# Kernel optimization log

Hardware: AMD Instinct MI355X
Metric: run time of the kernel (lower is better)

The kernel has to match this reference:

```python
import jax, jax.numpy as jnp
import numpy as np

NUM_CAPSULE = 128   # must equal steps (seq_len) for the reshape in the original code
DIM_CAPSULE = 64
ROUTINGS = 3
EPS = 1e-7          # K.epsilon()


def pos_emb(x):
    """Sinusoidal position embedding added to x over its last two dims [..., S, D].
    Matches the Keras code: evens use sin(pos/10000^(2k/D)), odds use cos with the
    same frequency (odds-1 == 2k), interleaved via stack+reshape."""
    S, D = x.shape[-2], x.shape[-1]
    pos = jnp.arange(S, dtype=x.dtype)[:, None]                      # [S,1]
    inv_freq = 1.0 / jnp.power(10000.0, (2.0 * jnp.arange(D // 2, dtype=x.dtype)) / D)
    ang = pos * inv_freq[None, :]                                    # [S, D/2]
    pe = jnp.stack([jnp.sin(ang), jnp.cos(ang)], axis=-1).reshape(S, D)
    return x + pe


def squash(s):
    ss = jnp.sum(s * s, axis=-1, keepdims=True)
    scale = ss / (1.0 + ss) / jnp.sqrt(ss + EPS)
    return scale * s


def setup_inputs() -> dict:
    key = jax.random.key(0)
    k1, k2 = jax.random.split(key)
    B, steps, in_dim = 32, 128, 256
    u_vecs = jax.random.normal(k1, (B, steps, in_dim), dtype=jnp.float32)
    mask = jnp.ones((B, steps), dtype=jnp.float32)
    # glorot_uniform for capsule kernel (1, in_dim, dim_capsule)
    lim = float(np.sqrt(6.0 / (in_dim + DIM_CAPSULE)))
    W = jax.random.uniform(k2, (1, in_dim, DIM_CAPSULE), jnp.float32, -lim, lim)
    return {"u_vecs": u_vecs, "mask": mask, "W": W}


def reference(u_vecs, mask, W):
    B, steps, in_dim = u_vecs.shape
    N, D = NUM_CAPSULE, DIM_CAPSULE  # N == steps by construction
    # share_weights branch: tile W across steps, permute, add PE, flatten to a conv1d
    # kernel of width 1 -> a plain [in_dim, steps*D] projection matrix.
    tmp = jnp.transpose(jnp.broadcast_to(W, (steps, in_dim, D)), (1, 0, 2))  # [in_dim, steps, D]
    kernel = pos_emb(tmp).reshape(in_dim, steps * D)                          # [in_dim, steps*D]
    u_hat = jnp.einsum('bsi,io->bso', u_vecs, kernel)                         # [B, steps, steps*D]
    u_hat = pos_emb(u_hat)
    u_hat = u_hat.reshape(B, steps, N, D).transpose(0, 2, 1, 3)               # [B, N, In, D]
    b = jnp.zeros((B, N, steps), dtype=u_hat.dtype)                           # routing logits
    m = mask[:, None, :]                                                      # [B, 1, In]
    outputs = None
    for i in range(ROUTINGS):
        # softmax over the num_capsule axis (permute->softmax(-1)->permute in Keras)
        c = jax.nn.softmax(b, axis=1) * m                                     # [B, N, In]
        outputs = squash(jnp.einsum('bni,bnid->bnd', c, u_hat))               # [B, N, D]
        if i < ROUTINGS - 1:
            b = jnp.einsum('bnd,bnid->bni', outputs, u_hat)                   # agreement
    return outputs
```

## Files before the change

### kernel.cpp

```cpp
#include <hip/hip_runtime.h>
#include <math.h>

#define NB 32
#define NS 128
#define NI 256
#define NC 128
#define ND 64

#define L4 9.210340371976184f

__global__ __launch_bounds__(256) void k_prep(const float* __restrict__ u,
                                              const float* __restrict__ W,
                                              float* __restrict__ M,
                                              float* __restrict__ U,
                                              float* __restrict__ PE1) {
    int blk = blockIdx.x;
    int t = threadIdx.x;
    if (blk < 1024) {
        int row = blk * 4 + (t >> 6);
        int d = t & 63;
        const float* ur = u + row * NI;
        float acc = 0.f, rs = 0.f;
#pragma unroll 4
        for (int i = 0; i < NI; ++i) {
            float v = ur[i];
            acc = fmaf(v, W[i * ND + d], acc);
            rs += v;
        }
        M[row * ND + d] = acc;
        if (d == 0) U[row] = rs;
    } else {
        int idx = (blk - 1024) * 256 + t;
        int n = idx >> 6, d = idx & 63;
        float ang = (float)n * __expf(-L4 * (float)(d >> 1) * (1.f / 32.f));
        float sv, cv;
        __sincosf(ang, &sv, &cv);
        PE1[idx] = (d & 1) ? cv : sv;
    }
}

__global__ __launch_bounds__(256, 4) void kR(const float* __restrict__ M,
                                             const float* __restrict__ U,
                                             const float* __restrict__ PE1,
                                             const float* __restrict__ cg,
                                             const float* __restrict__ mask,
                                             float* __restrict__ og,
                                             float* __restrict__ bl,
                                             int first, int last) {
    int bp = blockIdx.x;
    int n  = bp & 127;
    int b0 = (bp >> 7) * 2;
    int t  = threadIdx.x;

    __shared__ float4 redw[2][4][16];
    __shared__ float4 outs4[2][16];
    __shared__ float  tpar[2][2];
    __shared__ float  sc2[2][2];
    __shared__ float  red2[2][NS * 17];

    int dq = t & 15, sq = t >> 4;
    int s0 = sq * 8;

    const float* cr0 = first ? (mask + b0 * NS)
                             : (cg + ((size_t)(b0 * NC + n)) * NS);
    const float* cr1 = first ? (mask + (b0 + 1) * NS)
                             : (cg + ((size_t)((b0 + 1) * NC + n)) * NS);

    float4 c0a = *(const float4*)(cr0 + s0);
    float4 c0b = *(const float4*)(cr0 + s0 + 4);
    float4 c1a = *(const float4*)(cr1 + s0);
    float4 c1b = *(const float4*)(cr1 + s0 + 4);

    int k2 = n * 32 + dq * 2;
    float g0 = __expf(-L4 * (float)k2 * (1.f / 4096.f));
    float g1 = __expf(-L4 * (float)(k2 + 1) * (1.f / 4096.f));
    float sg0 = __sinf(g0), cg0 = __cosf(g0);
    float sg1 = __sinf(g1), cg1 = __cosf(g1);
    float sa = __sinf((float)s0 * g0), ca = __cosf((float)s0 * g0);
    float sb = __sinf((float)s0 * g1), cb = __cosf((float)s0 * g1);

    const float4* M4a = (const float4*)(M + (size_t)(b0 * NS) * ND) + dq;
    const float4* M4b = M4a + NS * 16;
    float4 va[8], vb[8];
    float4 acc0 = make_float4(0.f, 0.f, 0.f, 0.f);
    float4 acc1 = make_float4(0.f, 0.f, 0.f, 0.f);
#pragma unroll
    for (int i = 0; i < 8; ++i) {
        int s = s0 + i;
        float4 m0 = M4a[s * 16];
        float4 m1 = M4b[s * 16];
        float cc0 = (i < 4) ? ((const float*)&c0a)[i & 3] : ((const float*)&c0b)[i & 3];
        float cc1 = (i < 4) ? ((const float*)&c1a)[i & 3] : ((const float*)&c1b)[i & 3];
        float4 u0, u1;
        u0.x = m0.x + sa; u0.y = m0.y + ca; u0.z = m0.z + sb; u0.w = m0.w + cb;
        u1.x = m1.x + sa; u1.y = m1.y + ca; u1.z = m1.z + sb; u1.w = m1.w + cb;
        va[i] = u0; vb[i] = u1;
        acc0.x = fmaf(cc0, u0.x, acc0.x);
        acc0.y = fmaf(cc0, u0.y, acc0.y);
        acc0.z = fmaf(cc0, u0.z, acc0.z);
        acc0.w = fmaf(cc0, u0.w, acc0.w);
        acc1.x = fmaf(cc1, u1.x, acc1.x);
        acc1.y = fmaf(cc1, u1.y, acc1.y);
        acc1.z = fmaf(cc1, u1.z, acc1.z);
        acc1.w = fmaf(cc1, u1.w, acc1.w);
        float nsa = fmaf(sa, cg0, ca * sg0);
        float nca = fmaf(ca, cg0, -sa * sg0);
        sa = nsa; ca = nca;
        float nsb = fmaf(sb, cg1, cb * sg1);
        float ncb = fmaf(cb, cg1, -sb * sg1);
        sb = nsb; cb = ncb;
    }
#pragma unroll
    for (int o = 16; o <= 32; o <<= 1) {
        acc0.x += __shfl_xor(acc0.x, o); acc0.y += __shfl_xor(acc0.y, o);
        acc0.z += __shfl_xor(acc0.z, o); acc0.w += __shfl_xor(acc0.w, o);
        acc1.x += __shfl_xor(acc1.x, o); acc1.y += __shfl_xor(acc1.y, o);
        acc1.z += __shfl_xor(acc1.z, o); acc1.w += __shfl_xor(acc1.w, o);
    }
    if ((t & 48) == 0) {
        int w = t >> 6;
        redw[0][w][dq] = acc0;
        redw[1][w][dq] = acc1;
    }
    {
        int bh = t >> 7, s = t & 127;
        const float* cr = bh ? cr1 : cr0;
        float p = cr[s] * U[(b0 + bh) * NS + s];
#pragma unroll
        for (int o = 32; o > 0; o >>= 1) p += __shfl_xor(p, o);
        if ((t & 63) == 0) tpar[bh][(t >> 6) & 1] = p;
    }
    __syncthreads();

    if (t < 32) {
        int bh = t >> 4, q = t & 15;
        float4 r0 = redw[bh][0][q], r1 = redw[bh][1][q];
        float4 r2 = redw[bh][2][q], r3 = redw[bh][3][q];
        float4 o;
        o.x = r0.x + r1.x + r2.x + r3.x;
        o.y = r0.y + r1.y + r2.y + r3.y;
        o.z = r0.z + r1.z + r2.z + r3.z;
        o.w = r0.w + r1.w + r2.w + r3.w;
        float T2 = tpar[bh][0] + tpar[bh][1];
        float4 p14 = ((const float4*)PE1)[n * 16 + q];
        o.x = fmaf(p14.x, T2, o.x);
        o.y = fmaf(p14.y, T2, o.y);
        o.z = fmaf(p14.z, T2, o.z);
        o.w = fmaf(p14.w, T2, o.w);
        if (first) { o.x *= (1.f / 128.f); o.y *= (1.f / 128.f);
                     o.z *= (1.f / 128.f); o.w *= (1.f / 128.f); }
        outs4[bh][q] = o;
        float ssq = o.x * o.x + o.y * o.y + o.z * o.z + o.w * o.w;
        float ppu = o.x * p14.x + o.y * p14.y + o.z * p14.z + o.w * p14.w;
#pragma unroll
        for (int o2 = 1; o2 <= 8; o2 <<= 1) {
            ssq += __shfl_xor(ssq, o2);
            ppu += __shfl_xor(ppu, o2);
        }
        if (q == 0) {
            sc2[bh][0] = ssq / (1.f + ssq) * rsqrtf(ssq + 1e-7f);
            sc2[bh][1] = ppu;
        }
    }
    __syncthreads();

    if (last) {
        if (t < 32) {
            int bh = t >> 4, q = t & 15;
            float sc = sc2[bh][0];
            float4 o = outs4[bh][q];
            o.x *= sc; o.y *= sc; o.z *= sc; o.w *= sc;
            ((float4*)og)[((b0 + bh) * NC + n) * 16 + q] = o;
        }
        return;
    }

    float4 oa = outs4[0][dq], ob = outs4[1][dq];
#pragma unroll
    for (int i = 0; i < 8; ++i) {
        int s = s0 + i;
        float4 v0 = va[i], v1 = vb[i];
        red2[0][s * 17 + dq] = v0.x * oa.x + v0.y * oa.y + v0.z * oa.z + v0.w * oa.w;
        red2[1][s * 17 + dq] = v1.x * ob.x + v1.y * ob.y + v1.z * ob.z + v1.w * ob.w;
    }
    __syncthreads();
    {
        int bh = t >> 7, s = t & 127;
        const float* r = &red2[bh][s * 17];
        float sum = 0.f;
#pragma unroll
        for (int q = 0; q < 16; ++q) sum += r[q];
        bl[((b0 + bh) * NC + n) * NS + s] =
            sc2[bh][0] * (sum + sc2[bh][1] * U[(b0 + bh) * NS + s]);
    }
}

__global__ __launch_bounds__(256) void kS(const float* __restrict__ bl,
                                          const float* __restrict__ mask,
                                          float* __restrict__ c) {
    int blk = blockIdx.x;
    int b = blk >> 4, s0 = (blk & 15) * 8;
    int t = threadIdx.x;

    __shared__ float tl[NC][9];
    __shared__ float pr[32][9];
    __shared__ float ps[32][9];
    __shared__ float itot[8], msk[8];

    if (t < 8) msk[t] = mask[b * NS + s0 + t];
#pragma unroll
    for (int i = 0; i < 4; ++i) {
        int idx = i * 256 + t;
        int n = idx >> 3, si = idx & 7;
        tl[n][si] = bl[(b * NC + n) * NS + s0 + si];
    }
    __syncthreads();

    int si = t & 7, ch = t >> 3;
    float mx = -1e30f;
#pragma unroll
    for (int j = 0; j < 4; ++j) mx = fmaxf(mx, tl[ch * 4 + j][si]);
    pr[ch][si] = mx;
    __syncthreads();

    mx = pr[0][si];
#pragma unroll
    for (int jc = 1; jc < 32; ++jc) mx = fmaxf(mx, pr[jc][si]);
    float sm = 0.f;
#pragma unroll
    for (int j = 0; j < 4; ++j) {
        float e = __expf(tl[ch * 4 + j][si] - mx);
        tl[ch * 4 + j][si] = e;
        sm += e;
    }
    ps[ch][si] = sm;
    __syncthreads();

    if (t < 8) {
        float tot = 0.f;
#pragma unroll
        for (int jc = 0; jc < 32; ++jc) tot += ps[jc][t];
        itot[t] = msk[t] / tot;
    }
    __syncthreads();

#pragma unroll
    for (int i = 0; i < 4; ++i) {
        int idx = i * 256 + t;
        int n = idx >> 3, sj = idx & 7;
        c[(b * NC + n) * NS + s0 + sj] = tl[n][sj] * itot[sj];
    }
}

extern "C" void kernel_launch(void* const* d_in, const int* in_sizes, int n_in,
                              void* d_out, int out_size, void* d_ws, size_t ws_size,
                              hipStream_t stream) {
    const float* u    = (const float*)d_in[0];
    const float* mask = (const float*)d_in[1];
    const float* W    = (const float*)d_in[2];
    float* out = (float*)d_out;

    float* ws  = (float*)d_ws;
    float* M   = ws;
    float* U   = M + NB * NS * ND;
    float* PE1 = U + NB * NS;
    float* c   = PE1 + NC * ND;
    float* bl  = c + NB * NC * NS;

    k_prep<<<1056, 256, 0, stream>>>(u, W, M, U, PE1);

    kR<<<2048, 256, 0, stream>>>(M, U, PE1, c, mask, out, bl, 1, 0);
    kS<<<512, 256, 0, stream>>>(bl, mask, c);
    kR<<<2048, 256, 0, stream>>>(M, U, PE1, c, mask, out, bl, 0, 0);
    kS<<<512, 256, 0, stream>>>(bl, mask, c);
    kR<<<2048, 256, 0, stream>>>(M, U, PE1, c, mask, out, bl, 0, 1);
}
```

Before: 115.0 us.

## Fuse routing softmax into routing kernel and transpose logits layout

```diff
diff --git a/kernel.cpp b/kernel.cpp
--- a/kernel.cpp
+++ b/kernel.cpp
@@ -42,35 +42,57 @@
 __global__ __launch_bounds__(256, 4) void kR(const float* __restrict__ M,
                                              const float* __restrict__ U,
                                              const float* __restrict__ PE1,
-                                             const float* __restrict__ cg,
                                              const float* __restrict__ mask,
+                                             const float* __restrict__ blr,
+                                             float* __restrict__ blw,
                                              float* __restrict__ og,
-                                             float* __restrict__ bl,
                                              int first, int last) {
     int bp = blockIdx.x;
     int n  = bp & 127;
     int b0 = (bp >> 7) * 2;
     int t  = threadIdx.x;
 
+    __shared__ float  cs[2][NS];
     __shared__ float4 redw[2][4][16];
     __shared__ float4 outs4[2][16];
     __shared__ float  tpar[2][2];
     __shared__ float  sc2[2][2];
     __shared__ float  red2[2][NS * 17];
 
+    {
+        int bh = t >> 7, s = t & 127;
+        int b = b0 + bh;
+        float uu = U[b * NS + s];
+        float cv;
+        if (first) {
+            cv = mask[b * NS + s];
+        } else {
+            const float4* row = (const float4*)(blr + ((size_t)(b * NS + s)) * NC);
+            float mx = -1e30f;
+#pragma unroll 8
+            for (int i = 0; i < 32; ++i) {
+                float4 v = row[i];
+                mx = fmaxf(mx, fmaxf(fmaxf(v.x, v.y), fmaxf(v.z, v.w)));
+            }
+            float den = 0.f;
+#pragma unroll 8
+            for (int i = 0; i < 32; ++i) {
+                float4 v = row[i];
+                den += __expf(v.x - mx) + __expf(v.y - mx) +
+                       __expf(v.z - mx) + __expf(v.w - mx);
+            }
+            float blv = blr[((size_t)(b * NS + s)) * NC + n];
+            cv = __expf(blv - mx) * mask[b * NS + s] / den;
+        }
+        cs[bh][s] = cv;
+        float p = cv * uu;
+#pragma unroll
+        for (int o = 32; o > 0; o >>= 1) p += __shfl_xor(p, o);
+        if ((t & 63) == 0) tpar[bh][(t >> 6) & 1] = p;
+    }
+
     int dq = t & 15, sq = t >> 4;
     int s0 = sq * 8;
-
-    const float* cr0 = first ? (mask + b0 * NS)
-                             : (cg + ((size_t)(b0 * NC + n)) * NS);
-    const float* cr1 = first ? (mask + (b0 + 1) * NS)
-                             : (cg + ((size_t)((b0 + 1) * NC + n)) * NS);
-
-    float4 c0a = *(const float4*)(cr0 + s0);
-    float4 c0b = *(const float4*)(cr0 + s0 + 4);
-    float4 c1a = *(const float4*)(cr1 + s0);
-    float4 c1b = *(const float4*)(cr1 + s0 + 4);
-
     int k2 = n * 32 + dq * 2;
     float g0 = __expf(-L4 * (float)k2 * (1.f / 4096.f));
     float g1 = __expf(-L4 * (float)(k2 + 1) * (1.f / 4096.f));
@@ -78,6 +100,7 @@
     float sg1 = __sinf(g1), cg1 = __cosf(g1);
     float sa = __sinf((float)s0 * g0), ca = __cosf((float)s0 * g0);
     float sb = __sinf((float)s0 * g1), cb = __cosf((float)s0 * g1);
+    __syncthreads();
 
     const float4* M4a = (const float4*)(M + (size_t)(b0 * NS) * ND) + dq;
     const float4* M4b = M4a + NS * 16;
@@ -89,8 +112,7 @@
         int s = s0 + i;
         float4 m0 = M4a[s * 16];
         float4 m1 = M4b[s * 16];
-        float cc0 = (i < 4) ? ((const float*)&c0a)[i & 3] : ((const float*)&c0b)[i & 3];
-        float cc1 = (i < 4) ? ((const float*)&c1a)[i & 3] : ((const float*)&c1b)[i & 3];
+        float cc0 = cs[0][s], cc1 = cs[1][s];
         float4 u0, u1;
         u0.x = m0.x + sa; u0.y = m0.y + ca; u0.z = m0.z + sb; u0.w = m0.w + cb;
         u1.x = m1.x + sa; u1.y = m1.y + ca; u1.z = m1.z + sb; u1.w = m1.w + cb;
@@ -121,14 +143,6 @@
         int w = t >> 6;
         redw[0][w][dq] = acc0;
         redw[1][w][dq] = acc1;
-    }
-    {
-        int bh = t >> 7, s = t & 127;
-        const float* cr = bh ? cr1 : cr0;
-        float p = cr[s] * U[(b0 + bh) * NS + s];
-#pragma unroll
-        for (int o = 32; o > 0; o >>= 1) p += __shfl_xor(p, o);
-        if ((t & 63) == 0) tpar[bh][(t >> 6) & 1] = p;
     }
     __syncthreads();
 
@@ -186,69 +200,13 @@
     __syncthreads();
     {
         int bh = t >> 7, s = t & 127;
+        int b = b0 + bh;
         const float* r = &red2[bh][s * 17];
         float sum = 0.f;
 #pragma unroll
         for (int q = 0; q < 16; ++q) sum += r[q];
-        bl[((b0 + bh) * NC + n) * NS + s] =
-            sc2[bh][0] * (sum + sc2[bh][1] * U[(b0 + bh) * NS + s]);
-    }
-}
-
-__global__ __launch_bounds__(256) void kS(const float* __restrict__ bl,
-                                          const float* __restrict__ mask,
-                                          float* __restrict__ c) {
-    int blk = blockIdx.x;
-    int b = blk >> 4, s0 = (blk & 15) * 8;
-    int t = threadIdx.x;
-
-    __shared__ float tl[NC][9];
-    __shared__ float pr[32][9];
-    __shared__ float ps[32][9];
-    __shared__ float itot[8], msk[8];
-
-    if (t < 8) msk[t] = mask[b * NS + s0 + t];
-#pragma unroll
-    for (int i = 0; i < 4; ++i) {
-        int idx = i * 256 + t;
-        int n = idx >> 3, si = idx & 7;
-        tl[n][si] = bl[(b * NC + n) * NS + s0 + si];
-    }
-    __syncthreads();
-
-    int si = t & 7, ch = t >> 3;
-    float mx = -1e30f;
-#pragma unroll
-    for (int j = 0; j < 4; ++j) mx = fmaxf(mx, tl[ch * 4 + j][si]);
-    pr[ch][si] = mx;
-    __syncthreads();
-
-    mx = pr[0][si];
-#pragma unroll
-    for (int jc = 1; jc < 32; ++jc) mx = fmaxf(mx, pr[jc][si]);
-    float sm = 0.f;
-#pragma unroll
-    for (int j = 0; j < 4; ++j) {
-        float e = __expf(tl[ch * 4 + j][si] - mx);
-        tl[ch * 4 + j][si] = e;
-        sm += e;
-    }
-    ps[ch][si] = sm;
-    __syncthreads();
-
-    if (t < 8) {
-        float tot = 0.f;
-#pragma unroll
-        for (int jc = 0; jc < 32; ++jc) tot += ps[jc][t];
-        itot[t] = msk[t] / tot;
-    }
-    __syncthreads();
-
-#pragma unroll
-    for (int i = 0; i < 4; ++i) {
-        int idx = i * 256 + t;
-        int n = idx >> 3, sj = idx & 7;
-        c[(b * NC + n) * NS + s0 + sj] = tl[n][sj] * itot[sj];
+        blw[((size_t)(b * NS + s)) * NC + n] =
+            sc2[bh][0] * (sum + sc2[bh][1] * U[b * NS + s]);
     }
 }
 
@@ -264,14 +222,12 @@
     float* M   = ws;
     float* U   = M + NB * NS * ND;
     float* PE1 = U + NB * NS;
-    float* c   = PE1 + NC * ND;
-    float* bl  = c + NB * NC * NS;
+    float* bl0 = PE1 + NC * ND;
+    float* bl1 = bl0 + NB * NS * NC;
 
     k_prep<<<1056, 256, 0, stream>>>(u, W, M, U, PE1);
 
-    kR<<<2048, 256, 0, stream>>>(M, U, PE1, c, mask, out, bl, 1, 0);
-    kS<<<512, 256, 0, stream>>>(bl, mask, c);
-    kR<<<2048, 256, 0, stream>>>(M, U, PE1, c, mask, out, bl, 0, 0);
-    kS<<<512, 256, 0, stream>>>(bl, mask, c);
-    kR<<<2048, 256, 0, stream>>>(M, U, PE1, c, mask, out, bl, 0, 1);
+    kR<<<2048, 256, 0, stream>>>(M, U, PE1, mask, bl1, bl0, out, 1, 0);
+    kR<<<2048, 256, 0, stream>>>(M, U, PE1, mask, bl0, bl1, out, 0, 0);
+    kR<<<2048, 256, 0, stream>>>(M, U, PE1, mask, bl1, bl0, out, 0, 1);
 }
```

After: 239.7 us. 2.09x slower.
